# Kernel tuning notes

Hardware: AMD Instinct MI355X
Metric: run time of the kernel (lower is better)

## Reference

```python
import jax, jax.numpy as jnp
import numpy as np

EPS = 1e-5
DN = ('NCHW', 'OIHW', 'NCHW')

def _conv(x, w):
    return jax.lax.conv_general_dilated(x, w, (1, 1), 'VALID', dimension_numbers=DN)

def _bn4(x, g, b, m, v):
    # BatchNorm2d in eval mode, per-channel over NCHW
    inv = g / jnp.sqrt(v + EPS)
    return x * inv[None, :, None, None] + (b - m * inv)[None, :, None, None]

def _bn1(x, g, b, m, v):
    inv = g / jnp.sqrt(v + EPS)
    return x * inv[None, :] + (b - m * inv)[None, :]

def _hardtanh(x):
    return jnp.clip(x, -1.0, 1.0)

def _sign(x):
    return jnp.sign(x)

def _maxpool2(x):
    return jax.lax.reduce_window(x, -jnp.inf, jax.lax.max,
                                 (1, 1, 2, 2), (1, 1, 2, 2), 'VALID')

def setup_inputs() -> dict:
    key = jax.random.key(0)
    ks = jax.random.split(key, 20)
    B = 8192
    d = {
        'x': jax.random.normal(ks[0], (B, 8, 16, 16), jnp.float32),
        'w0': jax.random.normal(ks[1], (32, 8, 3, 3), jnp.float32) * 0.1,
        'b0': jax.random.normal(ks[2], (32,), jnp.float32) * 0.1,
        'g1': jax.random.uniform(ks[3], (32,), jnp.float32, 0.5, 1.5),
        'be1': jax.random.normal(ks[4], (32,), jnp.float32) * 0.1,
        'm1': jax.random.normal(ks[5], (32,), jnp.float32) * 0.1,
        'v1': jax.random.uniform(ks[6], (32,), jnp.float32, 0.5, 1.5),
        'w2': jax.random.normal(ks[7], (32, 32, 3, 3), jnp.float32) * 0.1,
        'g2': jax.random.uniform(ks[8], (32,), jnp.float32, 0.5, 1.5),
        'be2': jax.random.normal(ks[9], (32,), jnp.float32) * 0.1,
        'm2': jax.random.normal(ks[10], (32,), jnp.float32) * 0.1,
        'v2': jax.random.uniform(ks[11], (32,), jnp.float32, 0.5, 1.5),
        'w_fc': jax.random.normal(ks[12], (516, 1152), jnp.float32) * 0.03,
        'g3': jax.random.uniform(ks[13], (516,), jnp.float32, 0.5, 1.5),
        'be3': jax.random.normal(ks[14], (516,), jnp.float32) * 0.1,
        'm3': jax.random.normal(ks[15], (516,), jnp.float32) * 0.1,
        'v3': jax.random.uniform(ks[16], (516,), jnp.float32, 0.5, 1.5),
        'w_last': jax.random.normal(ks[17], (10, 516), jnp.float32) * 0.05,
        'b_last': jax.random.normal(ks[18], (10,), jnp.float32) * 0.05,
    }
    return d

def reference(x, w0, b0, g1, be1, m1, v1, w2, g2, be2, m2, v2,
              w_fc, g3, be3, m3, v3, w_last, b_last):
    # initial float conv + BN + Hardtanh
    h = _conv(x, w0) + b0[None, :, None, None]          # [B,32,14,14]
    h = _hardtanh(_bn4(h, g1, be1, m1, v1))
    # binarized conv (sign(input), sign(weight), no bias)
    h = _conv(_sign(h), _sign(w2))                      # [B,32,12,12]
    h = _hardtanh(_bn4(h, g2, be2, m2, v2))
    h = _maxpool2(h)                                    # [B,32,6,6]
    # dropout is identity in eval mode
    h = h.reshape(h.shape[0], -1)                       # [B,1152]
    # binarized linear (no bias)
    h = _sign(h) @ _sign(w_fc).T                        # [B,516]
    h = _hardtanh(_bn1(h, g3, be3, m3, v3))
    return h @ w_last.T + b_last[None, :]               # [B,10]
```

## Files before the change

### kernel.cpp

```cpp
#include <hip/hip_runtime.h>
#include <cstdint>

#define EPSF 1e-5f

typedef __attribute__((ext_vector_type(8))) short short8;
typedef __attribute__((ext_vector_type(4))) float f32x4;
typedef __attribute__((ext_vector_type(4))) unsigned int u32x4;

__device__ inline uint32_t bf16rne(float x) {
    uint32_t u = __builtin_bit_cast(uint32_t, x);
    return (u + 0x7fffu + ((u >> 16) & 1u)) >> 16;
}
__device__ inline float bf16f(uint32_t b) {
    return __builtin_bit_cast(float, b << 16);
}

__global__ __launch_bounds__(256) void prep_kernel(
    const float* __restrict__ w2, const float* __restrict__ wfc,
    const float* __restrict__ g3, const float* __restrict__ be3,
    const float* __restrict__ m3, const float* __restrict__ v3,
    const float* __restrict__ wlast,
    const float* __restrict__ w0, const float* __restrict__ b0,
    const float* __restrict__ g1, const float* __restrict__ be1,
    const float* __restrict__ m1, const float* __restrict__ v1,
    uint32_t* __restrict__ w2bits, uint32_t* __restrict__ wfcb,
    float* __restrict__ inv3p, float* __restrict__ sh3p, float* __restrict__ wlt,
    uint32_t* __restrict__ bfrag, float2* __restrict__ bn1c)
{
    int id = blockIdx.x * 256 + threadIdx.x;
    if (id < 288) {
        int co = id / 9, r = id % 9;
        uint32_t b = 0;
        for (int ci = 0; ci < 32; ci++)
            b |= (uint32_t)(w2[(co * 32 + ci) * 9 + r] < 0.f) << ci;
        w2bits[id] = b;
        return;
    }
    id -= 288;
    if (id < 36 * 576) {
        int j = id / 36, pos = id % 36;
        uint32_t b = 0;
        if (j < 516) {
            const float* row = wfc + j * 1152 + pos;
            for (int c = 0; c < 32; c++)
                b |= (uint32_t)(row[c * 36] < 0.f) << c;
        }
        wfcb[pos * 576 + j] = b;
        return;
    }
    id -= 36 * 576;
    if (id < 576) {
        float iv = 0.f, sh = 0.f;
        if (id < 516) {
            iv = g3[id] / sqrtf(__fadd_rn(v3[id], EPSF));
            sh = __fsub_rn(be3[id], __fmul_rn(m3[id], iv));
        }
        inv3p[id] = iv; sh3p[id] = sh;
        return;
    }
    id -= 576;
    if (id < 5760) {
        int k = id / 576, j = id % 576;
        wlt[id] = (j < 516) ? wlast[k * 516 + j] : 0.f;
        return;
    }
    id -= 5760;
    if (id < 768) {
        int L = id / 12, r = id % 12;
        int nt = r / 6, s = (r % 6) / 2, h = r & 1;
        int g = L >> 4, n = L & 15;
        int tap = 4 * s + g;
        uint32_t d[4] = {0, 0, 0, 0};
        if (tap < 9) {
            int co = nt * 16 + n;
            for (int j2 = 0; j2 < 4; j2++) {
                float wa = w0[co * 72 + (2 * j2) * 9 + tap];
                float wb = w0[co * 72 + (2 * j2 + 1) * 9 + tap];
                uint32_t ha = bf16rne(wa), hb = bf16rne(wb);
                uint32_t va, vb;
                if (h == 0) { va = ha; vb = hb; }
                else { va = bf16rne(wa - bf16f(ha)); vb = bf16rne(wb - bf16f(hb)); }
                d[j2] = va | (vb << 16);
            }
        }
        *(u32x4*)(bfrag + id * 4) = (u32x4){d[0], d[1], d[2], d[3]};
        return;
    }
    id -= 768;
    if (id < 32) {
        float iv = g1[id] / sqrtf(__fadd_rn(v1[id], EPSF));
        float sh = __fsub_rn(be1[id], __fmul_rn(m1[id], iv));
        float off = __fadd_rn(__fmul_rn(b0[id], iv), sh);
        bn1c[id] = make_float2(iv, off);
    }
}

__device__ __noinline__ bool recheck_sign(const float* __restrict__ xim,
                                          const float* __restrict__ w0,
                                          int py, int px, int co,
                                          float ivc, float offc)
{
    double ad = 0.0;
    for (int ci = 0; ci < 8; ci++)
        for (int ky = 0; ky < 3; ky++)
            for (int kx = 0; kx < 3; kx++)
                ad = fma((double)xim[ci * 256 + (py + ky) * 16 + px + kx],
                         (double)w0[co * 72 + ci * 9 + ky * 3 + kx], ad);
    return (ad * (double)ivc + (double)offc) < 0.0;
}

__global__ __launch_bounds__(128, 4) void convA(
    const float* __restrict__ x, const float* __restrict__ w0,
    const uint32_t* __restrict__ bfrag, const float2* __restrict__ bn1c,
    uint32_t* __restrict__ s1bits)
{
    __shared__ __align__(16) char simg[9216];

    const int t = threadIdx.x;
    const int wv = t >> 6, lane = t & 63;
    const int img = blockIdx.x;
    const float* xim = x + img * 2048;
    char* hib = simg;
    char* lob = simg + 4608;

    const int g = lane >> 4;
    const int n = lane & 15;

    short8 Bh[2][3], Bl[2][3];
    {
        const uint32_t* bb = bfrag + lane * 48;
        #pragma unroll
        for (int nt = 0; nt < 2; nt++)
            #pragma unroll
            for (int s = 0; s < 3; s++) {
                Bh[nt][s] = *(const short8*)(bb + (nt * 6 + s * 2) * 4);
                Bl[nt][s] = *(const short8*)(bb + (nt * 6 + s * 2 + 1) * 4);
            }
    }
    const float2 bnA = bn1c[n], bnB = bn1c[16 + n];

    #pragma unroll
    for (int qq = 0; qq < 2; qq++) {
        int pos = lane + 64 * (2 * wv + qq);
        uint32_t hw[4], lw[4];
        #pragma unroll
        for (int j2 = 0; j2 < 4; j2++) {
            float a = xim[(2 * j2) * 256 + pos];
            float b = xim[(2 * j2 + 1) * 256 + pos];
            uint32_t ha = bf16rne(a), hb = bf16rne(b);
            uint32_t la = bf16rne(a - bf16f(ha)), lb = bf16rne(b - bf16f(hb));
            hw[j2] = ha | (hb << 16);
            lw[j2] = la | (lb << 16);
        }
        *(u32x4*)(hib + pos * 16) = (u32x4){hw[0], hw[1], hw[2], hw[3]};
        *(u32x4*)(lob + pos * 16) = (u32x4){lw[0], lw[1], lw[2], lw[3]};
    }
    if (lane < 32) {
        char* gp = (wv == 0) ? hib : lob;
        *(u32x4*)(gp + (256 + lane) * 16) = (u32x4){0, 0, 0, 0};
    }

    int koff[3];
    #pragma unroll
    for (int s = 0; s < 3; s++) {
        int tap = 4 * s + g;
        koff[s] = (tap < 9) ? ((tap / 3) * 16 + (tap % 3)) * 16 : 0;
    }

    __syncthreads();

    uint32_t* outb = s1bits + img * 196;

    for (int tile = wv; tile < 13; tile += 2) {
        int posA = tile * 16 + n;
        int pyA = posA / 14, pxA = posA - pyA * 14;
        int sl = (pyA * 16 + pxA) * 16;

        f32x4 acc0 = {0.f, 0.f, 0.f, 0.f}, acc1 = {0.f, 0.f, 0.f, 0.f};
        #pragma unroll
        for (int s = 0; s < 3; s++) {
            short8 Ah = *(const short8*)(hib + sl + koff[s]);
            short8 Al = *(const short8*)(lob + sl + koff[s]);
            acc0 = __builtin_amdgcn_mfma_f32_16x16x32_bf16(Al, Bh[0][s], acc0, 0, 0, 0);
            acc0 = __builtin_amdgcn_mfma_f32_16x16x32_bf16(Ah, Bl[0][s], acc0, 0, 0, 0);
            acc0 = __builtin_amdgcn_mfma_f32_16x16x32_bf16(Ah, Bh[0][s], acc0, 0, 0, 0);
            acc1 = __builtin_amdgcn_mfma_f32_16x16x32_bf16(Al, Bh[1][s], acc1, 0, 0, 0);
            acc1 = __builtin_amdgcn_mfma_f32_16x16x32_bf16(Ah, Bl[1][s], acc1, 0, 0, 0);
            acc1 = __builtin_amdgcn_mfma_f32_16x16x32_bf16(Ah, Bh[1][s], acc1, 0, 0, 0);
        }

        #pragma unroll
        for (int r = 0; r < 4; r++) {
            int pos = tile * 16 + 4 * g + r;
            float yv0 = fmaf(acc0[r], bnA.x, bnA.y);
            float yv1 = fmaf(acc1[r], bnB.x, bnB.y);
            bool bit0, bit1;
            if (__builtin_expect(pos < 196 && fabsf(yv0) < 3e-4f, 0)) {
                int py = pos / 14, px = pos - py * 14;
                bit0 = recheck_sign(xim, w0, py, px, n, bnA.x, bnA.y);
            } else bit0 = (yv0 < 0.f);
            if (__builtin_expect(pos < 196 && fabsf(yv1) < 3e-4f, 0)) {
                int py = pos / 14, px = pos - py * 14;
                bit1 = recheck_sign(xim, w0, py, px, 16 + n, bnB.x, bnB.y);
            } else bit1 = (yv1 < 0.f);
            unsigned long long m0 = __ballot(bit0);
            unsigned long long m1 = __ballot(bit1);
            uint32_t word = (uint32_t)((m0 >> (16 * g)) & 0xffffull)
                          | ((uint32_t)((m1 >> (16 * g)) & 0xffffull) << 16);
            if (n == 0 && pos < 196) outb[pos] = word;
        }
    }
}

__global__ __launch_bounds__(256) void convB(
    const uint32_t* __restrict__ s1bits, const uint32_t* __restrict__ w2bits,
    const float* __restrict__ g2, const float* __restrict__ be2,
    const float* __restrict__ m2, const float* __restrict__ v2,
    uint32_t* __restrict__ fcin)
{
    __shared__ uint32_t s1l[4][196];
    const int t = threadIdx.x, wid = t >> 6, lane = t & 63;
    const int img = blockIdx.x * 4 + wid;

    for (int i = lane; i < 196; i += 64) s1l[wid][i] = s1bits[img * 196 + i];

    const int c = lane & 31, h = lane >> 5;
    uint32_t wr[9];
    #pragma unroll
    for (int k = 0; k < 9; k++) wr[k] = w2bits[c * 9 + k];
    float ivv = g2[c] / sqrtf(__fadd_rn(v2[c], EPSF));
    float shv = __fsub_rn(be2[c], __fmul_rn(m2[c], ivv));
    __syncthreads();

    const uint32_t* s1w = s1l[wid];
    uint32_t* outp = fcin + img * 36;

    for (int yy = 0; yy < 3; yy++) {
        const int y2 = yy + 3 * h;
        const int rbase = 2 * y2 * 14;
        uint32_t win[4][4];
        #pragma unroll
        for (int rr = 0; rr < 4; rr++) {
            uint2 a = *(const uint2*)&s1w[rbase + rr * 14];
            uint2 b = *(const uint2*)&s1w[rbase + rr * 14 + 2];
            win[rr][0] = a.x; win[rr][1] = a.y; win[rr][2] = b.x; win[rr][3] = b.y;
        }
        for (int x2 = 0; x2 < 6; x2++) {
            if (x2 > 0) {
                #pragma unroll
                for (int rr = 0; rr < 4; rr++) {
                    win[rr][0] = win[rr][2]; win[rr][1] = win[rr][3];
                    uint2 b = *(const uint2*)&s1w[rbase + rr * 14 + 2 * x2 + 2];
                    win[rr][2] = b.x; win[rr][3] = b.y;
                }
            }
            int mx = -10000;
            #pragma unroll
            for (int dy = 0; dy < 2; dy++)
                #pragma unroll
                for (int dx = 0; dx < 2; dx++) {
                    int p = 0;
                    #pragma unroll
                    for (int ky = 0; ky < 3; ky++)
                        #pragma unroll
                        for (int kx = 0; kx < 3; kx++)
                            p += __popc(win[dy + ky][dx + kx] ^ wr[ky * 3 + kx]);
                    mx = max(mx, 288 - 2 * p);
                }
            float yv = __fadd_rn(__fmul_rn((float)mx, ivv), shv);
            unsigned long long mb = __ballot(yv < 0.f);
            int pos = y2 * 6 + x2;
            if (lane == 0)  outp[pos] = (uint32_t)mb;
            if (lane == 32) outp[pos] = (uint32_t)(mb >> 32);
        }
    }
}

__global__ __launch_bounds__(256) void fcC(
    const uint32_t* __restrict__ fcin, const uint32_t* __restrict__ wfcb,
    const float* __restrict__ inv3p, const float* __restrict__ sh3p,
    const float* __restrict__ wlt, const float* __restrict__ blast,
    float* __restrict__ out)
{
    __shared__ uint32_t l_in[288];
    const int t = threadIdx.x, wid = t >> 6, lane = t & 63;

    for (int i = t; i < 288; i += 256) l_in[i] = fcin[blockIdx.x * 288 + i];
    __syncthreads();

    const int b0i = blockIdx.x * 8 + wid * 2;
    const uint32_t* in0 = &l_in[wid * 72];

    int pc0[9], pc1[9];
    #pragma unroll
    for (int q = 0; q < 9; q++) { pc0[q] = 0; pc1[q] = 0; }

    for (int w = 0; w < 36; w++) {
        uint32_t i0 = in0[w], i1 = in0[36 + w];
        const uint32_t* wf = wfcb + w * 576 + lane;
        #pragma unroll
        for (int q = 0; q < 9; q++) {
            uint32_t f = wf[q * 64];
            pc0[q] += __popc(i0 ^ f);
            pc1[q] += __popc(i1 ^ f);
        }
    }

    float oa[2][10];
    #pragma unroll
    for (int b = 0; b < 2; b++)
        #pragma unroll
        for (int k = 0; k < 10; k++) oa[b][k] = 0.f;

    #pragma unroll
    for (int q = 0; q < 9; q++) {
        int j = lane + 64 * q;
        float ivv = inv3p[j], shv = sh3p[j];
        float t0 = fminf(1.f, fmaxf(-1.f, __fadd_rn(__fmul_rn((float)(1152 - 2 * pc0[q]), ivv), shv)));
        float t1 = fminf(1.f, fmaxf(-1.f, __fadd_rn(__fmul_rn((float)(1152 - 2 * pc1[q]), ivv), shv)));
        #pragma unroll
        for (int k = 0; k < 10; k++) {
            float wv = wlt[k * 576 + j];
            oa[0][k] = fmaf(t0, wv, oa[0][k]);
            oa[1][k] = fmaf(t1, wv, oa[1][k]);
        }
    }

    #pragma unroll
    for (int m = 1; m < 64; m <<= 1)
        #pragma unroll
        for (int b = 0; b < 2; b++)
            #pragma unroll
            for (int k = 0; k < 10; k++)
                oa[b][k] += __shfl_xor(oa[b][k], m, 64);

    if (lane == 0) {
        for (int b = 0; b < 2; b++)
            for (int k = 0; k < 10; k++)
                out[(b0i + b) * 10 + k] = oa[b][k] + blast[k];
    }
}

extern "C" void kernel_launch(void* const* d_in, const int* in_sizes, int n_in,
                              void* d_out, int out_size, void* d_ws, size_t ws_size,
                              hipStream_t stream)
{
    (void)in_sizes; (void)n_in; (void)out_size; (void)ws_size;
    const float* x     = (const float*)d_in[0];
    const float* w0    = (const float*)d_in[1];
    const float* b0    = (const float*)d_in[2];
    const float* g1    = (const float*)d_in[3];
    const float* be1   = (const float*)d_in[4];
    const float* m1    = (const float*)d_in[5];
    const float* v1    = (const float*)d_in[6];
    const float* w2    = (const float*)d_in[7];
    const float* g2    = (const float*)d_in[8];
    const float* be2   = (const float*)d_in[9];
    const float* m2    = (const float*)d_in[10];
    const float* v2    = (const float*)d_in[11];
    const float* wfc   = (const float*)d_in[12];
    const float* g3    = (const float*)d_in[13];
    const float* be3   = (const float*)d_in[14];
    const float* m3    = (const float*)d_in[15];
    const float* v3    = (const float*)d_in[16];
    const float* wlast = (const float*)d_in[17];
    const float* blast = (const float*)d_in[18];

    char* ws = (char*)d_ws;
    uint32_t* s1bits = (uint32_t*)(ws);
    uint32_t* fcin   = (uint32_t*)(ws + 6422528);
    uint32_t* w2bits = (uint32_t*)(ws + 7602176);
    uint32_t* wfcb   = (uint32_t*)(ws + 7603328);
    float*    inv3p  = (float*)(ws + 7686272);
    float*    sh3p   = (float*)(ws + 7688576);
    float*    wlt    = (float*)(ws + 7690880);
    uint32_t* bfrag  = (uint32_t*)(ws + 7713920);
    float2*   bn1c   = (float2*)(ws + 7726208);

    prep_kernel<<<110, 256, 0, stream>>>(w2, wfc, g3, be3, m3, v3, wlast,
                                         w0, b0, g1, be1, m1, v1,
                                         w2bits, wfcb, inv3p, sh3p, wlt,
                                         bfrag, bn1c);
    convA<<<8192, 128, 0, stream>>>(x, w0, bfrag, bn1c, s1bits);
    convB<<<2048, 256, 0, stream>>>(s1bits, w2bits, g2, be2, m2, v2, fcin);
    fcC<<<1024, 256, 0, stream>>>(fcin, wfcb, inv3p, sh3p, wlt, blast, (float*)d_out);
}
```

Before: 218.5 us.

## Fuse binarized conv2 and maxpool into first conv kernel via shared memory

Merges convA and convB into one kernel. The sign bitmap of the first conv now stays in shared memory and is consumed directly by the XNOR-popcount conv, pool and sign stage, so the s1bits round trip through global memory and one kernel launch are removed. The popcount work is remapped across the block's two waves (each wave takes three pooled rows, each half-wave takes three columns). It also raises wave priority around the MFMA section. The costs are an extra block-wide barrier, a per-block reload of w2 and BN parameters, and the popcount stage now running at the 128-thread block occupancy.

```diff
diff --git a/kernel.cpp b/kernel.cpp
--- a/kernel.cpp
+++ b/kernel.cpp
@@ -109,12 +109,16 @@
     return (ad * (double)ivc + (double)offc) < 0.0;
 }
 
-__global__ __launch_bounds__(128, 4) void convA(
+__global__ __launch_bounds__(128, 4) void convAB(
     const float* __restrict__ x, const float* __restrict__ w0,
     const uint32_t* __restrict__ bfrag, const float2* __restrict__ bn1c,
-    uint32_t* __restrict__ s1bits)
+    const uint32_t* __restrict__ w2bits,
+    const float* __restrict__ g2, const float* __restrict__ be2,
+    const float* __restrict__ m2, const float* __restrict__ v2,
+    uint32_t* __restrict__ fcin)
 {
     __shared__ __align__(16) char simg[9216];
+    __shared__ __align__(8) uint32_t s1l[196];
 
     const int t = threadIdx.x;
     const int wv = t >> 6, lane = t & 63;
@@ -169,14 +173,13 @@
 
     __syncthreads();
 
-    uint32_t* outb = s1bits + img * 196;
-
     for (int tile = wv; tile < 13; tile += 2) {
         int posA = tile * 16 + n;
         int pyA = posA / 14, pxA = posA - pyA * 14;
         int sl = (pyA * 16 + pxA) * 16;
 
         f32x4 acc0 = {0.f, 0.f, 0.f, 0.f}, acc1 = {0.f, 0.f, 0.f, 0.f};
+        __builtin_amdgcn_s_setprio(1);
         #pragma unroll
         for (int s = 0; s < 3; s++) {
             short8 Ah = *(const short8*)(hib + sl + koff[s]);
@@ -188,6 +191,7 @@
             acc1 = __builtin_amdgcn_mfma_f32_16x16x32_bf16(Ah, Bl[1][s], acc1, 0, 0, 0);
             acc1 = __builtin_amdgcn_mfma_f32_16x16x32_bf16(Ah, Bh[1][s], acc1, 0, 0, 0);
         }
+        __builtin_amdgcn_s_setprio(0);
 
         #pragma unroll
         for (int r = 0; r < 4; r++) {
@@ -207,71 +211,60 @@
             unsigned long long m1 = __ballot(bit1);
             uint32_t word = (uint32_t)((m0 >> (16 * g)) & 0xffffull)
                           | ((uint32_t)((m1 >> (16 * g)) & 0xffffull) << 16);
-            if (n == 0 && pos < 196) outb[pos] = word;
-        }
-    }
-}
-
-__global__ __launch_bounds__(256) void convB(
-    const uint32_t* __restrict__ s1bits, const uint32_t* __restrict__ w2bits,
-    const float* __restrict__ g2, const float* __restrict__ be2,
-    const float* __restrict__ m2, const float* __restrict__ v2,
-    uint32_t* __restrict__ fcin)
-{
-    __shared__ uint32_t s1l[4][196];
-    const int t = threadIdx.x, wid = t >> 6, lane = t & 63;
-    const int img = blockIdx.x * 4 + wid;
-
-    for (int i = lane; i < 196; i += 64) s1l[wid][i] = s1bits[img * 196 + i];
-
-    const int c = lane & 31, h = lane >> 5;
-    uint32_t wr[9];
-    #pragma unroll
-    for (int k = 0; k < 9; k++) wr[k] = w2bits[c * 9 + k];
-    float ivv = g2[c] / sqrtf(__fadd_rn(v2[c], EPSF));
-    float shv = __fsub_rn(be2[c], __fmul_rn(m2[c], ivv));
+            if (n == 0 && pos < 196) s1l[pos] = word;
+        }
+    }
+
     __syncthreads();
-
-    const uint32_t* s1w = s1l[wid];
-    uint32_t* outp = fcin + img * 36;
-
-    for (int yy = 0; yy < 3; yy++) {
-        const int y2 = yy + 3 * h;
-        const int rbase = 2 * y2 * 14;
-        uint32_t win[4][4];
-        #pragma unroll
-        for (int rr = 0; rr < 4; rr++) {
-            uint2 a = *(const uint2*)&s1w[rbase + rr * 14];
-            uint2 b = *(const uint2*)&s1w[rbase + rr * 14 + 2];
-            win[rr][0] = a.x; win[rr][1] = a.y; win[rr][2] = b.x; win[rr][3] = b.y;
-        }
-        for (int x2 = 0; x2 < 6; x2++) {
-            if (x2 > 0) {
+    __builtin_amdgcn_sched_barrier(0);
+
+    {
+        const int c = lane & 31, h = lane >> 5;
+        uint32_t wr[9];
+        #pragma unroll
+        for (int k = 0; k < 9; k++) wr[k] = w2bits[c * 9 + k];
+        float ivv = g2[c] / sqrtf(__fadd_rn(v2[c], EPSF));
+        float shv = __fsub_rn(be2[c], __fmul_rn(m2[c], ivv));
+        uint32_t* outp = fcin + img * 36;
+        const int cb0 = 6 * h;
+
+        for (int yy = 0; yy < 3; yy++) {
+            const int y2 = 3 * wv + yy;
+            const int rbase = 2 * y2 * 14;
+            uint32_t win[4][4];
+            #pragma unroll
+            for (int rr = 0; rr < 4; rr++) {
+                uint2 a = *(const uint2*)&s1l[rbase + rr * 14 + cb0];
+                uint2 b = *(const uint2*)&s1l[rbase + rr * 14 + cb0 + 2];
+                win[rr][0] = a.x; win[rr][1] = a.y; win[rr][2] = b.x; win[rr][3] = b.y;
+            }
+            for (int step = 0; step < 3; step++) {
+                if (step > 0) {
+                    #pragma unroll
+                    for (int rr = 0; rr < 4; rr++) {
+                        win[rr][0] = win[rr][2]; win[rr][1] = win[rr][3];
+                        uint2 b = *(const uint2*)&s1l[rbase + rr * 14 + cb0 + 2 * step + 2];
+                        win[rr][2] = b.x; win[rr][3] = b.y;
+                    }
+                }
+                int mx = -10000;
                 #pragma unroll
-                for (int rr = 0; rr < 4; rr++) {
-                    win[rr][0] = win[rr][2]; win[rr][1] = win[rr][3];
-                    uint2 b = *(const uint2*)&s1w[rbase + rr * 14 + 2 * x2 + 2];
-                    win[rr][2] = b.x; win[rr][3] = b.y;
-                }
+                for (int dy = 0; dy < 2; dy++)
+                    #pragma unroll
+                    for (int dx = 0; dx < 2; dx++) {
+                        int p = 0;
+                        #pragma unroll
+                        for (int ky = 0; ky < 3; ky++)
+                            #pragma unroll
+                            for (int kx = 0; kx < 3; kx++)
+                                p += __popc(win[dy + ky][dx + kx] ^ wr[ky * 3 + kx]);
+                        mx = max(mx, 288 - 2 * p);
+                    }
+                float yv = __fadd_rn(__fmul_rn((float)mx, ivv), shv);
+                unsigned long long mb = __ballot(yv < 0.f);
+                if (lane == 0)  outp[y2 * 6 + step]     = (uint32_t)mb;
+                if (lane == 32) outp[y2 * 6 + step + 3] = (uint32_t)(mb >> 32);
             }
-            int mx = -10000;
-            #pragma unroll
-            for (int dy = 0; dy < 2; dy++)
-                #pragma unroll
-                for (int dx = 0; dx < 2; dx++) {
-                    int p = 0;
-                    #pragma unroll
-                    for (int ky = 0; ky < 3; ky++)
-                        #pragma unroll
-                        for (int kx = 0; kx < 3; kx++)
-                            p += __popc(win[dy + ky][dx + kx] ^ wr[ky * 3 + kx]);
-                    mx = max(mx, 288 - 2 * p);
-                }
-            float yv = __fadd_rn(__fmul_rn((float)mx, ivv), shv);
-            unsigned long long mb = __ballot(yv < 0.f);
-            int pos = y2 * 6 + x2;
-            if (lane == 0)  outp[pos] = (uint32_t)mb;
-            if (lane == 32) outp[pos] = (uint32_t)(mb >> 32);
         }
     }
 }
@@ -367,7 +360,6 @@
     const float* blast = (const float*)d_in[18];
 
     char* ws = (char*)d_ws;
-    uint32_t* s1bits = (uint32_t*)(ws);
     uint32_t* fcin   = (uint32_t*)(ws + 6422528);
     uint32_t* w2bits = (uint32_t*)(ws + 7602176);
     uint32_t* wfcb   = (uint32_t*)(ws + 7603328);
@@ -381,7 +373,7 @@
                                          w0, b0, g1, be1, m1, v1,
                                          w2bits, wfcb, inv3p, sh3p, wlt,
                                          bfrag, bn1c);
-    convA<<<8192, 128, 0, stream>>>(x, w0, bfrag, bn1c, s1bits);
-    convB<<<2048, 256, 0, stream>>>(s1bits, w2bits, g2, be2, m2, v2, fcin);
+    convAB<<<8192, 128, 0, stream>>>(x, w0, bfrag, bn1c,
+                                     w2bits, g2, be2, m2, v2, fcin);
     fcC<<<1024, 256, 0, stream>>>(fcin, wfcb, inv3p, sh3p, wlt, blast, (float*)d_out);
 }
```

New measurement: 217.2 us. Within noise of the previous version (-0.6%).
